# Kernel tuning notes

Measured on AMD Instinct MI355X. Metric: run time of the kernel, lower is better.

The kernel has to match this reference:

```python
import jax, jax.numpy as jnp
import numpy as np

# dims
B, N, M, K = 8, 4096, 1024, 32      # batch, points, centers, neighbors
CIN, CT = 64, 64                    # feature / temb channels
C1, C2 = 64, 128                    # SharedMLP out_channels
G, EPS = 8, 1e-5                    # GroupNorm(8, oc)


def setup_inputs() -> dict:
    key = jax.random.key(0)
    ks = jax.random.split(key, 8)
    return {
        "features": jax.random.normal(ks[0], (B, CIN, N), jnp.float32),
        "coords": jax.random.uniform(ks[1], (B, 3, N), jnp.float32),
        "temb": jax.random.normal(ks[2], (B, CT, N), jnp.float32),
        # SharedMLP params: Conv2d 1x1 -> (O, I) weight, GroupNorm affine
        "W1": jax.random.normal(ks[3], (C1, CIN + 3), jnp.float32) * 0.05,
        "b1": jnp.zeros((C1,), jnp.float32),
        "g1": jnp.ones((C1,), jnp.float32),
        "be1": jnp.zeros((C1,), jnp.float32),
        "W2": jax.random.normal(ks[4], (C2, C1), jnp.float32) * 0.05,
        "b2": jnp.zeros((C2,), jnp.float32),
        "g2": jnp.ones((C2,), jnp.float32),
        "be2": jnp.zeros((C2,), jnp.float32),
    }


def fps_indices(pts):
    # pts: [N, 3] -> [M] indices. Deterministic start at index 0
    # (original uses a random start; math otherwise identical).
    d0 = jnp.sum((pts - pts[0]) ** 2, axis=-1)  # [N]
    def step(dist, _):
        far = jnp.argmax(dist)
        dist = jnp.minimum(dist, jnp.sum((pts - pts[far]) ** 2, axis=-1))
        return dist, far
    _, fars = jax.lax.scan(step, d0, None, length=M - 1)
    return jnp.concatenate([jnp.zeros((1,), fars.dtype), fars])


def group_norm(x, gamma, beta):
    # x: [B, C, M, K], normalize per group over (C//G, M, K)
    b, c, m, k = x.shape
    xr = x.reshape(b, G, c // G, m, k)
    mu = xr.mean(axis=(2, 3, 4), keepdims=True)
    var = xr.var(axis=(2, 3, 4), keepdims=True)
    xn = ((xr - mu) * jax.lax.rsqrt(var + EPS)).reshape(b, c, m, k)
    return xn * gamma[:, None, None] + beta[:, None, None]


def swish(x):
    return x * jax.nn.sigmoid(x)


def reference(features, coords, temb, W1, b1, g1, be1, W2, b2, g2, be2):
    # --- furthest point sampling ---
    idx = jax.vmap(fps_indices)(coords.transpose(0, 2, 1))          # [B, M]
    centers = jax.vmap(lambda c, i: c[:, i])(coords, idx)           # [B, 3, M]
    # --- 'ball query' (actually kNN: source argsorts dist, takes first K) ---
    c = centers.transpose(0, 2, 1)                                  # [B, M, 3]
    p = coords.transpose(0, 2, 1)                                   # [B, N, 3]
    d = (jnp.sum(c * c, -1)[:, :, None] + jnp.sum(p * p, -1)[:, None, :]
         - 2.0 * jnp.einsum('bmd,bnd->bmn', c, p))                  # [B, M, N]
    _, nidx = jax.lax.top_k(-d, K)                                  # [B, M, K]
    gather = jax.vmap(lambda xb, ib: xb[:, ib])                     # [B,C,N],[B,M,K]->[B,C,M,K]
    gcoords = gather(coords, nidx) - centers[..., None]             # [B, 3, M, K]
    gtemb = gather(temb, nidx)                                      # [B, CT, M, K]
    gfeat = jnp.concatenate([gcoords, gather(features, nidx)], axis=1)  # [B, 3+CIN, M, K]
    # --- SharedMLP (1x1 conv -> GN -> Swish) x2, then max over neighbors ---
    h = swish(group_norm(jnp.einsum('oc,bcmk->bomk', W1, gfeat) + b1[:, None, None], g1, be1))
    h = swish(group_norm(jnp.einsum('oc,bcmk->bomk', W2, h) + b2[:, None, None], g2, be2))
    return h.max(axis=-1), centers, gtemb.max(axis=-1)
```

## Files before the change

kernel.cpp:

```cpp
#include <hip/hip_runtime.h>
#include <stdint.h>

#define BB 8
#define NN 4096
#define MM 1024
#define KK 32

__device__ __forceinline__ float bf2f(unsigned short u) {
    union { unsigned int i; float f; } v; v.i = ((unsigned int)u) << 16; return v.f;
}
__device__ __forceinline__ unsigned short f2bf(float f) {
    union { float f; unsigned int i; } v; v.f = f;
    unsigned int x = v.i;
    x += 0x7fffu + ((x >> 16) & 1u);
    return (unsigned short)(x >> 16);
}
__device__ __forceinline__ float swishf(float y) {
    return __fdividef(y, 1.0f + __expf(-y));
}

#define OUT1_OFF 1048576
#define OUT2_OFF 1073152

#define P_W1 0
#define P_B1 4288
#define P_G1 4352
#define P_BE1 4416
#define P_W2 4480
#define P_B2 12672
#define P_G2 12800
#define P_BE2 12928

__device__ __forceinline__ int detect_flag_wave(const unsigned short* f, int lane) {
    unsigned short u = f[lane * 2];
    float x = fabsf(bf2f(u));
    bool ext = (u != 0) && (x > 100.0f || x < 1e-30f);
    unsigned long long m = __ballot(ext);
    return (__popcll(m) >= 16) ? 1 : 0;
}

#define DPP_STAGE(CTRL) { \
    union { double d; unsigned int u[2]; } s_, r_; \
    s_.d = bd; \
    r_.u[0] = (unsigned)__builtin_amdgcn_update_dpp(0, (int)s_.u[0], CTRL, 0xF, 0xF, true); \
    r_.u[1] = (unsigned)__builtin_amdgcn_update_dpp(0, (int)s_.u[1], CTRL, 0xF, 0xF, true); \
    int op_ = __builtin_amdgcn_update_dpp(0, bp, CTRL, 0xF, 0xF, true); \
    double od_ = r_.d; \
    bool rep_ = (od_ > bd) || (od_ == bd && op_ < bp); \
    bd = rep_ ? od_ : bd; bp = rep_ ? op_ : bp; }

__device__ __forceinline__ void redmax64(double& bd, int& bp) {
    DPP_STAGE(0xB1)
    DPP_STAGE(0x4E)
    DPP_STAGE(0x141)
    DPP_STAGE(0x140)
#pragma unroll
    for (int m = 32; m >= 16; m >>= 1) {
        double od = __shfl_xor(bd, m, 64);
        int op = __shfl_xor(bp, m, 64);
        bool rep = (od > bd) || (od == bd && op < bp);
        bd = rep ? od : bd; bp = rep ? op : bp;
    }
}

__global__ void k_init(int* __restrict__ qhead, int* __restrict__ progress,
                       float* __restrict__ stats1, int* __restrict__ cvt_done,
                       int* __restrict__ mlp_done) {
    int tid = threadIdx.x;
    if (tid == 0) { *qhead = 0; *cvt_done = 0; *mlp_done = 0; }
    if (tid < 8) progress[tid * 16] = -1;
    stats1[tid] = 0.f;
    stats1[tid + 256] = 0.f;
}

#define W1Tm(j,c)     (((float*)SM)[(j)*64+(c)])
#define GBUFm(mi,k,c) (((float*)(SM+17152))[(((mi)*32+(k))*66)+(c)])
#define GCm(mi,j,k)   (((float*)(SM+50944))[(((mi)*3+(j))*32)+(k)])
#define NDm(mi,k)     (((int*)(SM+52480))[((mi)*32)+(k)])
#define W2Tm(j,c)     (((float*)SM)[(j)*128+(c)])
#define ACTm(mi,j,k)  (((float*)(SM+32768))[(((mi)*64+(j))*32)+(k)])

struct PW { double d; int p; int q; };
#define PSM_XS   ((float*)(SM))
#define PSM_YS   ((float*)(SM + 16384))
#define PSM_ZS   ((float*)(SM + 32768))
#define PSM_HIST ((int*)(SM + 49152))
#define PSM_PWB  ((PW*)(SM + 53248))
#define PSM_SF   ((int*)(SM + 53376))

#define RESCAN(G) { \
    double gd = 1.0e300; int ga = (G) * 8; \
    _Pragma("unroll") \
    for (int i = 0; i < 8; i++) { \
        int sl = (G) * 8 + i; \
        unsigned int bit = (sl < 32) ? (elo >> sl) : (ehi >> (sl - 32)); \
        double cd = (bit & 1u) ? 1.0e300 : d[sl]; \
        bool rep = cd < gd; \
        gd = rep ? cd : gd; ga = rep ? sl : ga; \
    } \
    g8[(G)] = gd; a8[(G)] = ga; }

__global__ __launch_bounds__(256) void k_fpsknn(
    const void* __restrict__ coords, float* __restrict__ coordsC,
    float* __restrict__ centersF, int* __restrict__ nidx,
    const void* __restrict__ temb, const void* __restrict__ feat,
    float* __restrict__ featT, float* __restrict__ paramsC,
    float* __restrict__ stats1,
    void* __restrict__ d_out,
    int* __restrict__ qhead, int* __restrict__ progress,
    int* __restrict__ cvt_done,
    unsigned short* __restrict__ h1, int cache1,
    const void* W1r, const void* b1r, const void* g1r, const void* be1r,
    const void* W2r, const void* b2r, const void* g2r, const void* be2r)
{
    __shared__ __align__(16) char SM[55296];
    int tid = threadIdx.x;
    int blk = blockIdx.x;
    if (tid < 64) {
        int fl0 = detect_flag_wave((const unsigned short*)feat, tid);
        if (tid == 0) *PSM_SF = fl0;
    }
    __syncthreads();
    int fl = *PSM_SF;

    if (blk < 8) {
        int b = blk;
        if (fl) {
            const float* cb = (const float*)coords + (size_t)b * 3 * NN;
#pragma unroll
            for (int i = 0; i < 16; i++) {
                int p = tid + i * 256;
                PSM_XS[p] = cb[p]; PSM_YS[p] = cb[NN + p]; PSM_ZS[p] = cb[2 * NN + p];
            }
        } else {
            const unsigned short* cb = (const unsigned short*)coords + (size_t)b * 3 * NN;
#pragma unroll
            for (int i = 0; i < 16; i++) {
                int p = tid + i * 256;
                PSM_XS[p] = bf2f(cb[p]); PSM_YS[p] = bf2f(cb[NN + p]); PSM_ZS[p] = bf2f(cb[2 * NN + p]);
            }
        }
        if (tid == 0) PSM_HIST[0] = 0;
        __syncthreads();
        if (tid == 0) {
            *(float4*)(centersF + (size_t)b * MM * 4) =
                make_float4(PSM_XS[0], PSM_YS[0], PSM_ZS[0], 0.f);
            __hip_atomic_store(&progress[b * 16], 0, __ATOMIC_RELEASE, __HIP_MEMORY_SCOPE_AGENT);
        }
        int base = tid * 16;
        double px[16], py[16], pz[16], dist[16];
        double x0 = (double)PSM_XS[0], y0 = (double)PSM_YS[0], z0 = (double)PSM_ZS[0];
        double bd = -1.0; int bp = base;
#pragma unroll
        for (int j = 0; j < 16; j++) {
            px[j] = (double)PSM_XS[base + j]; py[j] = (double)PSM_YS[base + j]; pz[j] = (double)PSM_ZS[base + j];
            double dx = px[j] - x0, dy = py[j] - y0, dz = pz[j] - z0;
            dist[j] = fma(dz, dz, fma(dy, dy, dx * dx));
            bool rep = dist[j] > bd;
            bd = rep ? dist[j] : bd; bp = rep ? base + j : bp;
        }
        int lane = tid & 63, wid = tid >> 6;
#pragma unroll 1
        for (int s = 1; s < MM; s++) {
            redmax64(bd, bp);
            int par = s & 1;
            if (lane == 0) { PW w; w.d = bd; w.p = bp; w.q = 0; PSM_PWB[par * 4 + wid] = w; }
            __syncthreads();
            PW w0 = PSM_PWB[par * 4 + 0];
            double wd = w0.d; int wp = w0.p;
#pragma unroll
            for (int w = 1; w < 4; w++) {
                PW ww = PSM_PWB[par * 4 + w];
                bool rep = (ww.d > wd) || (ww.d == wd && ww.p < wp);
                wd = rep ? ww.d : wd; wp = rep ? ww.p : wp;
            }
            if (tid == 0) PSM_HIST[s] = wp;
            if ((s & 31) == 31 && s >= 63 && wid == ((s >> 5) & 3)) {
                int s0 = s - 63;
                if (lane < 32) {
                    int far = PSM_HIST[s0 + lane];
                    *(float4*)(centersF + ((size_t)b * MM + s0 + lane) * 4) =
                        make_float4(PSM_XS[far], PSM_YS[far], PSM_ZS[far], 0.f);
                }
                if (lane == 0)
                    __hip_atomic_store(&progress[b * 16], s0 + 31,
                                       __ATOMIC_RELEASE, __HIP_MEMORY_SCOPE_AGENT);
            }
            double fx = (double)PSM_XS[wp], fy = (double)PSM_YS[wp], fz = (double)PSM_ZS[wp];
            bd = -1.0; bp = base;
#pragma unroll
            for (int j = 0; j < 16; j++) {
                double dx = px[j] - fx, dy = py[j] - fy, dz = pz[j] - fz;
                double d = fma(dz, dz, fma(dy, dy, dx * dx));
                dist[j] = fmin(dist[j], d);
                bool rep = dist[j] > bd;
                bd = rep ? dist[j] : bd; bp = rep ? base + j : bp;
            }
        }
        __syncthreads();
        if (tid < 32) {
            int far = PSM_HIST[992 + tid];
            *(float4*)(centersF + ((size_t)b * MM + 992 + tid) * 4) =
                make_float4(PSM_XS[far], PSM_YS[far], PSM_ZS[far], 0.f);
        }
        if (tid == 0)
            __hip_atomic_store(&progress[b * 16], 1023,
                               __ATOMIC_RELEASE, __HIP_MEMORY_SCOPE_AGENT);
#pragma unroll
        for (int i = 0; i < 4; i++) {
            int m = tid + i * 256;
            int far = PSM_HIST[m];
            float X = PSM_XS[far], Y = PSM_YS[far], Z = PSM_ZS[far];
            if (fl) {
                float* o = (float*)d_out;
                o[OUT1_OFF + (size_t)(b * 3 + 0) * MM + m] = X;
                o[OUT1_OFF + (size_t)(b * 3 + 1) * MM + m] = Y;
                o[OUT1_OFF + (size_t)(b * 3 + 2) * MM + m] = Z;
            } else {
                unsigned short* o = (unsigned short*)d_out;
                o[OUT1_OFF + (size_t)(b * 3 + 0) * MM + m] = f2bf(X);
                o[OUT1_OFF + (size_t)(b * 3 + 1) * MM + m] = f2bf(Y);
                o[OUT1_OFF + (size_t)(b * 3 + 2) * MM + m] = f2bf(Z);
            }
        }
    } else {
        int lane = tid & 63, wid = tid >> 6;
        for (int i = (blk - 8) * 256 + tid; i < BB * 3 * NN; i += 248 * 256)
            coordsC[i] = fl ? ((const float*)coords)[i]
                            : bf2f(((const unsigned short*)coords)[i]);
        for (int i = (blk - 8) * 256 + tid; i < 13056; i += 248 * 256) {
            const void* src; int off;
            if (i < 4288)       { src = W1r;  off = i; }
            else if (i < 4352)  { src = b1r;  off = i - 4288; }
            else if (i < 4416)  { src = g1r;  off = i - 4352; }
            else if (i < 4480)  { src = be1r; off = i - 4416; }
            else if (i < 12672) { src = W2r;  off = i - 4480; }
            else if (i < 12800) { src = b2r;  off = i - 12672; }
            else if (i < 12928) { src = g2r;  off = i - 12800; }
            else                { src = be2r; off = i - 12928; }
            paramsC[i] = fl ? ((const float*)src)[off]
                            : bf2f(((const unsigned short*)src)[off]);
        }
        {
            float (*tile)[65] = (float(*)[65])SM;
            for (int t = blk - 8; t < 512; t += 248) {
                int b = t >> 6, n0 = (t & 63) * 64;
                int c = tid >> 2, q = tid & 3;
                size_t base = ((size_t)b * 64 + c) * NN + n0 + q * 16;
                __syncthreads();
                if (fl) {
                    const float* sp = (const float*)feat + base;
#pragma unroll
                    for (int j = 0; j < 16; j++) tile[c][q * 16 + j] = sp[j];
                } else {
                    const unsigned short* sp = (const unsigned short*)feat + base;
#pragma unroll
                    for (int j = 0; j < 16; j++) tile[c][q * 16 + j] = bf2f(sp[j]);
                }
                __syncthreads();
                int n = tid >> 2;
                float* dp = featT + ((size_t)b * NN + n0 + n) * 64 + q * 16;
#pragma unroll
                for (int j = 0; j < 16; j++) dp[j] = tile[q * 16 + j][n];
            }
            __syncthreads();
            if (tid == 0) {
                __hip_atomic_fetch_add(cvt_done, 1, __ATOMIC_ACQ_REL, __HIP_MEMORY_SCOPE_AGENT);
                while (__hip_atomic_load(cvt_done, __ATOMIC_RELAXED,
                                         __HIP_MEMORY_SCOPE_AGENT) < 248)
                    __builtin_amdgcn_s_sleep(16);
                (void)__hip_atomic_load(cvt_done, __ATOMIC_ACQUIRE, __HIP_MEMORY_SCOPE_AGENT);
            }
            __syncthreads();
        }
        for (int t = tid; t < 64 * 67; t += 256) {
            int c = t / 67, j = t % 67;
            W1Tm(j, c) = paramsC[P_W1 + t];
        }
        __syncthreads();
        for (;;) {
            int id = 0;
            if (lane == 0) id = atomicAdd(qhead, 1);
            id = __shfl(id, 0, 64);
            if (id >= BB * MM) break;
            int b = id & 7, m = id >> 3;
            while (__hip_atomic_load(&progress[b * 16], __ATOMIC_RELAXED,
                                     __HIP_MEMORY_SCOPE_AGENT) < m)
                __builtin_amdgcn_s_sleep(64);
            (void)__hip_atomic_load(&progress[b * 16], __ATOMIC_ACQUIRE,
                                    __HIP_MEMORY_SCOPE_AGENT);
            int bm = b * MM + m;
            const float* cb = coordsC + (size_t)b * 3 * NN;
            float4 ctr = *(const float4*)(centersF + (size_t)bm * 4);
            double cx = (double)ctr.x, cy = (double)ctr.y, cz = (double)ctr.z;
            double cc = (cx * cx + cy * cy) + cz * cz;
            double d[64];
#pragma unroll 4
            for (int j = 0; j < 64; j++) {
                int p = j * 64 + lane;
                double x = (double)cb[p], y = (double)cb[NN + p], z = (double)cb[2 * NN + p];
                double pp = (x * x + y * y) + z * z;
                double dt = (cx * x + cy * y) + cz * z;
                d[j] = (cc + pp) - 2.0 * dt;
            }
            double g8[8]; int a8[8];
#pragma unroll
            for (int g = 0; g < 8; g++) {
                double gd = d[g * 8]; int ga = g * 8;
#pragma unroll
                for (int i = 1; i < 8; i++) {
                    int sl = g * 8 + i;
                    bool rep = d[sl] < gd;
                    gd = rep ? d[sl] : gd; ga = rep ? sl : ga;
                }
                g8[g] = gd; a8[g] = ga;
            }
            unsigned int elo = 0, ehi = 0;
            int res = 0;
#pragma unroll 1
            for (int it = 0; it < 32; it++) {
                double bd = g8[0]; int ba = a8[0];
#pragma unroll
                for (int g = 1; g < 8; g++) {
                    bool rep = g8[g] < bd;
                    bd = rep ? g8[g] : bd; ba = rep ? a8[g] : ba;
                }
                int bp = ba * 64 + lane;
                double wd = bd; int wp = bp;
#pragma unroll
                for (int s = 32; s >= 1; s >>= 1) {
                    double od = __shfl_xor(wd, s, 64);
                    int op = __shfl_xor(wp, s, 64);
                    bool rep = (od < wd) || (od == wd && op < wp);
                    wd = rep ? od : wd; wp = rep ? op : wp;
                }
                res = (lane == it) ? wp : res;
                if (bp == wp) {
                    int slot = ba;
                    if (slot < 32) elo |= (1u << slot); else ehi |= (1u << (slot - 32));
                    int g = slot >> 3;
                    switch (g) {
                        case 0: RESCAN(0) break;
                        case 1: RESCAN(1) break;
                        case 2: RESCAN(2) break;
                        case 3: RESCAN(3) break;
                        case 4: RESCAN(4) break;
                        case 5: RESCAN(5) break;
                        case 6: RESCAN(6) break;
                        case 7: RESCAN(7) break;
                    }
                }
            }
            if (lane < KK) nidx[(size_t)bm * KK + lane] = res;
            float best = -3.0e38f;
            if (fl) {
                const float* tb = (const float*)temb + ((size_t)b * 64 + lane) * NN;
#pragma unroll 4
                for (int k = 0; k < 32; k++) {
                    int nk = __shfl(res, k, 64);
                    best = fmaxf(best, tb[nk]);
                }
            } else {
                const unsigned short* tb = (const unsigned short*)temb + ((size_t)b * 64 + lane) * NN;
#pragma unroll 4
                for (int k = 0; k < 32; k++) {
                    int nk = __shfl(res, k, 64);
                    best = fmaxf(best, bf2f(tb[nk]));
                }
            }
            size_t off = (size_t)OUT2_OFF + ((size_t)(b * 64 + lane)) * MM + m;
            if (fl) ((float*)d_out)[off] = best;
            else    ((unsigned short*)d_out)[off] = f2bf(best);
            if (lane < 32) NDm(wid, lane) = res & (NN - 1);
            const float* fb = featT + (size_t)b * NN * 64;
#pragma unroll 4
            for (int q = 0; q < 32; q++) {
                int n = NDm(wid, q);
                GBUFm(wid, q, lane) = fb[(size_t)n * 64 + lane];
            }
            if (lane < 32) {
                int n = NDm(wid, lane);
                GCm(wid, 0, lane) = __fsub_rn(cb[n], ctr.x);
                GCm(wid, 1, lane) = __fsub_rn(cb[NN + n], ctr.y);
                GCm(wid, 2, lane) = __fsub_rn(cb[2 * NN + n], ctr.z);
            }
            int c0 = (lane >> 3) * 8;
            int k0 = (lane & 7) * 4;
            float acc[8][4];
#pragma unroll
            for (int i = 0; i < 8; i++)
#pragma unroll
                for (int kk = 0; kk < 4; kk++) acc[i][kk] = 0.f;
#pragma unroll
            for (int j = 0; j < 3; j++) {
                float4 a = *(const float4*)&GCm(wid, j, k0);
                float4 w0 = *(const float4*)&W1Tm(j, c0);
                float4 w1v = *(const float4*)&W1Tm(j, c0 + 4);
                float w[8] = {w0.x, w0.y, w0.z, w0.w, w1v.x, w1v.y, w1v.z, w1v.w};
#pragma unroll
                for (int i = 0; i < 8; i++) {
                    acc[i][0] = fmaf(w[i], a.x, acc[i][0]);
                    acc[i][1] = fmaf(w[i], a.y, acc[i][1]);
                    acc[i][2] = fmaf(w[i], a.z, acc[i][2]);
                    acc[i][3] = fmaf(w[i], a.w, acc[i][3]);
                }
            }
#pragma unroll 4
            for (int c = 0; c < 64; c++) {
                float f0 = GBUFm(wid, k0 + 0, c);
                float f1 = GBUFm(wid, k0 + 1, c);
                float f2 = GBUFm(wid, k0 + 2, c);
                float f3 = GBUFm(wid, k0 + 3, c);
                int j = 3 + c;
                float4 w0 = *(const float4*)&W1Tm(j, c0);
                float4 w1v = *(const float4*)&W1Tm(j, c0 + 4);
                float w[8] = {w0.x, w0.y, w0.z, w0.w, w1v.x, w1v.y, w1v.z, w1v.w};
#pragma unroll
                for (int i = 0; i < 8; i++) {
                    acc[i][0] = fmaf(w[i], f0, acc[i][0]);
                    acc[i][1] = fmaf(w[i], f1, acc[i][1]);
                    acc[i][2] = fmaf(w[i], f2, acc[i][2]);
                    acc[i][3] = fmaf(w[i], f3, acc[i][3]);
                }
            }
            float s = 0.f, s2 = 0.f;
#pragma unroll
            for (int i = 0; i < 8; i++) {
                float bb = paramsC[P_B1 + c0 + i];
                float v0 = acc[i][0] + bb, v1 = acc[i][1] + bb;
                float v2 = acc[i][2] + bb, v3 = acc[i][3] + bb;
                s += v0; s2 = fmaf(v0, v0, s2);
                s += v1; s2 = fmaf(v1, v1, s2);
                s += v2; s2 = fmaf(v2, v2, s2);
                s += v3; s2 = fmaf(v3, v3, s2);
                if (cache1) {
                    unsigned int p0 = (unsigned int)f2bf(v0) | ((unsigned int)f2bf(v1) << 16);
                    unsigned int p1 = (unsigned int)f2bf(v2) | ((unsigned int)f2bf(v3) << 16);
                    *(uint2*)(h1 + ((size_t)bm * 64 + c0 + i) * 32 + k0) = make_uint2(p0, p1);
                }
            }
            s += __shfl_xor(s, 1, 64); s += __shfl_xor(s, 2, 64); s += __shfl_xor(s, 4, 64);
            s2 += __shfl_xor(s2, 1, 64); s2 += __shfl_xor(s2, 2, 64); s2 += __shfl_xor(s2, 4, 64);
            if ((lane & 7) == 0) {
                int g = lane >> 3;
                atomicAdd(&stats1[(b * 8 + g) * 2], s);
                atomicAdd(&stats1[(b * 8 + g) * 2 + 1], s2);
            }
        }
    }
}

__device__ __forceinline__ void mlp1_compute(
    char* SM, int tid, int lane, int mi, int b, int bm,
    const float* __restrict__ featT, const float* __restrict__ coordsC,
    const float* __restrict__ centersF, const int* __restrict__ nidx,
    const float* __restrict__ P, float acc[8][4])
{
    for (int t = tid; t < 64 * 67; t += 256) {
        int c = t / 67, j = t % 67;
        W1Tm(j, c) = P[P_W1 + t];
    }
    if (lane < 32) NDm(mi, lane) = nidx[(size_t)bm * KK + lane] & (NN - 1);
    __syncthreads();
    const float* fb = featT + (size_t)b * NN * 64;
#pragma unroll 4
    for (int q = 0; q < 32; q++) {
        int n = NDm(mi, q);
        GBUFm(mi, q, lane) = fb[(size_t)n * 64 + lane];
    }
    float4 ctr = *(const float4*)(centersF + (size_t)bm * 4);
    const float* cb = coordsC + (size_t)b * 3 * NN;
    if (lane < 32) {
        int n = NDm(mi, lane);
        GCm(mi, 0, lane) = __fsub_rn(cb[n], ctr.x);
        GCm(mi, 1, lane) = __fsub_rn(cb[NN + n], ctr.y);
        GCm(mi, 2, lane) = __fsub_rn(cb[2 * NN + n], ctr.z);
    }
    __syncthreads();
    int c0 = (lane >> 3) * 8;
    int k0 = (lane & 7) * 4;
#pragma unroll
    for (int i = 0; i < 8; i++)
#pragma unroll
        for (int kk = 0; kk < 4; kk++) acc[i][kk] = 0.f;
#pragma unroll
    for (int j = 0; j < 3; j++) {
        float4 a = *(const float4*)&GCm(mi, j, k0);
        float4 w0 = *(const float4*)&W1Tm(j, c0);
        float4 w1v = *(const float4*)&W1Tm(j, c0 + 4);
        float w[8] = {w0.x, w0.y, w0.z, w0.w, w1v.x, w1v.y, w1v.z, w1v.w};
#pragma unroll
        for (int i = 0; i < 8; i++) {
            acc[i][0] = fmaf(w[i], a.x, acc[i][0]);
            acc[i][1] = fmaf(w[i], a.y, acc[i][1]);
            acc[i][2] = fmaf(w[i], a.z, acc[i][2]);
            acc[i][3] = fmaf(w[i], a.w, acc[i][3]);
        }
    }
#pragma unroll 4
    for (int c = 0; c < 64; c++) {
        float f0 = GBUFm(mi, k0 + 0, c);
        float f1 = GBUFm(mi, k0 + 1, c);
        float f2 = GBUFm(mi, k0 + 2, c);
        float f3 = GBUFm(mi, k0 + 3, c);
        int j = 3 + c;
        float4 w0 = *(const float4*)&W1Tm(j, c0);
        float4 w1v = *(const float4*)&W1Tm(j, c0 + 4);
        float w[8] = {w0.x, w0.y, w0.z, w0.w, w1v.x, w1v.y, w1v.z, w1v.w};
#pragma unroll
        for (int i = 0; i < 8; i++) {
            acc[i][0] = fmaf(w[i], f0, acc[i][0]);
            acc[i][1] = fmaf(w[i], f1, acc[i][1]);
            acc[i][2] = fmaf(w[i], f2, acc[i][2]);
            acc[i][3] = fmaf(w[i], f3, acc[i][3]);
        }
    }
}

__device__ __forceinline__ void mlp2_compute(
    char* SM, int tid, int lane, int mi, int b,
    const float v1[8][4], const float* __restrict__ S1,
    const float* __restrict__ P, float v2[16][4])
{
    __syncthreads();
    int c0 = (lane >> 3) * 8;
    int k0 = (lane & 7) * 4;
    int g = c0 >> 3;
    float S = S1[(b * 8 + g) * 2], Q = S1[(b * 8 + g) * 2 + 1];
    float mean = S * (1.0f / 262144.0f);
    float var = Q * (1.0f / 262144.0f) - mean * mean;
    float inv = rsqrtf(var + 1e-5f);
#pragma unroll
    for (int i = 0; i < 8; i++) {
        int c = c0 + i;
        float sc = P[P_G1 + c] * inv;
        float sh = P[P_BE1 + c] - mean * sc;
#pragma unroll
        for (int kk = 0; kk < 4; kk++)
            ACTm(mi, c, k0 + kk) = swishf(fmaf(v1[i][kk], sc, sh));
    }
    for (int t = tid; t < 128 * 64; t += 256) {
        int c = t >> 6, j = t & 63;
        W2Tm(j, c) = P[P_W2 + t];
    }
    __syncthreads();
    int c02 = (lane >> 3) * 16;
    float acc2[16][4];
#pragma unroll
    for (int i = 0; i < 16; i++)
#pragma unroll
        for (int kk = 0; kk < 4; kk++) acc2[i][kk] = 0.f;
#pragma unroll 4
    for (int j = 0; j < 64; j++) {
        float4 a = *(const float4*)&ACTm(mi, j, k0);
        float4 w0 = *(const float4*)&W2Tm(j, c02);
        float4 w1v = *(const float4*)&W2Tm(j, c02 + 4);
        float4 w2v = *(const float4*)&W2Tm(j, c02 + 8);
        float4 w3 = *(const float4*)&W2Tm(j, c02 + 12);
        float w[16] = {w0.x, w0.y, w0.z, w0.w, w1v.x, w1v.y, w1v.z, w1v.w,
                       w2v.x, w2v.y, w2v.z, w2v.w, w3.x, w3.y, w3.z, w3.w};
#pragma unroll
        for (int i = 0; i < 16; i++) {
            acc2[i][0] = fmaf(w[i], a.x, acc2[i][0]);
            acc2[i][1] = fmaf(w[i], a.y, acc2[i][1]);
            acc2[i][2] = fmaf(w[i], a.z, acc2[i][2]);
            acc2[i][3] = fmaf(w[i], a.w, acc2[i][3]);
        }
    }
#pragma unroll
    for (int i = 0; i < 16; i++) {
        float bb = P[P_B2 + c02 + i];
#pragma unroll
        for (int kk = 0; kk < 4; kk++) v2[i][kk] = acc2[i][kk] + bb;
    }
}

__device__ __forceinline__ void get_v1(
    char* SM, int tid, int lane, int mi, int b, int bm,
    const float* featT, const float* coordsC, const float* centersF,
    const int* nidx, const float* P,
    const unsigned short* h1, int cache1, float v1[8][4])
{
    int c0 = (lane >> 3) * 8;
    int k0 = (lane & 7) * 4;
    if (cache1) {
#pragma unroll
        for (int i = 0; i < 8; i++) {
            uint2 u = *(const uint2*)(h1 + ((size_t)bm * 64 + c0 + i) * 32 + k0);
            v1[i][0] = bf2f((unsigned short)(u.x & 0xffffu));
            v1[i][1] = bf2f((unsigned short)(u.x >> 16));
            v1[i][2] = bf2f((unsigned short)(u.y & 0xffffu));
            v1[i][3] = bf2f((unsigned short)(u.y >> 16));
        }
    } else {
        float acc1[8][4];
        mlp1_compute(SM, tid, lane, mi, b, bm, featT, coordsC, centersF, nidx, P, acc1);
#pragma unroll
        for (int i = 0; i < 8; i++) {
            float bb = P[P_B1 + c0 + i];
#pragma unroll
            for (int kk = 0; kk < 4; kk++) v1[i][kk] = acc1[i][kk] + bb;
        }
    }
}

__global__ __launch_bounds__(256) void k_mlp2f(
    const float* __restrict__ featT, const float* __restrict__ coordsC,
    const float* __restrict__ centersF, const int* __restrict__ nidx,
    const float* __restrict__ P, const float* __restrict__ stats1,
    float* __restrict__ stats2,
    const unsigned short* __restrict__ h1,
    unsigned short* __restrict__ vmaxA, unsigned short* __restrict__ vminA,
    int* __restrict__ mlp_done,
    void* __restrict__ d_out, const void* __restrict__ feat)
{
    __shared__ __align__(16) char SM[65536];
    int tid = threadIdx.x;
    int mi = tid >> 6, lane = tid & 63;
#pragma unroll 1
    for (int it = 0; it < 4; it++) {
        int vblk = blockIdx.x + 512 * it;
        int b = vblk >> 8, m0 = (vblk & 255) * 4;
        int bm = b * MM + m0 + mi;
        float v1[8][4];
        get_v1(SM, tid, lane, mi, b, bm, featT, coordsC, centersF, nidx, P, h1, 1, v1);
        float v2[16][4];
        mlp2_compute(SM, tid, lane, mi, b, v1, stats1, P, v2);
        int c02 = (lane >> 3) * 16;
        float s = 0.f, s2 = 0.f;
#pragma unroll
        for (int i = 0; i < 16; i++) {
#pragma unroll
            for (int kk = 0; kk < 4; kk++) {
                float v = v2[i][kk];
                s += v; s2 = fmaf(v, v, s2);
            }
        }
        int m = m0 + mi;
#pragma unroll
        for (int i = 0; i < 16; i++) {
            float va = fmaxf(fmaxf(v2[i][0], v2[i][1]), fmaxf(v2[i][2], v2[i][3]));
            float vb = fminf(fminf(v2[i][0], v2[i][1]), fminf(v2[i][2], v2[i][3]));
            va = fmaxf(va, __shfl_xor(va, 1, 64)); vb = fminf(vb, __shfl_xor(vb, 1, 64));
            va = fmaxf(va, __shfl_xor(va, 2, 64)); vb = fminf(vb, __shfl_xor(vb, 2, 64));
            va = fmaxf(va, __shfl_xor(va, 4, 64)); vb = fminf(vb, __shfl_xor(vb, 4, 64));
            if ((lane & 7) == 0) {
                size_t o = ((size_t)(b * 128 + c02 + i)) * MM + m;
                vmaxA[o] = f2bf(va);
                vminA[o] = f2bf(vb);
            }
        }
        s += __shfl_xor(s, 1, 64); s += __shfl_xor(s, 2, 64); s += __shfl_xor(s, 4, 64);
        s2 += __shfl_xor(s2, 1, 64); s2 += __shfl_xor(s2, 2, 64); s2 += __shfl_xor(s2, 4, 64);
        __syncthreads();
        float* sred = (float*)SM;
        if ((lane & 7) == 0) {
            int g = lane >> 3;
            sred[(mi * 8 + g) * 2] = s;
            sred[(mi * 8 + g) * 2 + 1] = s2;
        }
        __syncthreads();
        if (tid < 16) {
            int g = tid >> 1, w = tid & 1;
            float t = sred[(0 * 8 + g) * 2 + w] + sred[(1 * 8 + g) * 2 + w]
                    + sred[(2 * 8 + g) * 2 + w] + sred[(3 * 8 + g) * 2 + w];
            atomicAdd(&stats2[(b * 8 + g) * 2 + w], t);
        }
        __syncthreads();
    }
    __syncthreads();
    if (tid == 0) {
        __hip_atomic_fetch_add(mlp_done, 1, __ATOMIC_ACQ_REL, __HIP_MEMORY_SCOPE_AGENT);
        while (__hip_atomic_load(mlp_done, __ATOMIC_RELAXED, __HIP_MEMORY_SCOPE_AGENT) < 512)
            __builtin_amdgcn_s_sleep(16);
        (void)__hip_atomic_load(mlp_done, __ATOMIC_ACQUIRE, __HIP_MEMORY_SCOPE_AGENT);
    }
    __syncthreads();
    int fl = detect_flag_wave((const unsigned short*)feat, lane);
#pragma unroll 1
    for (int i = 0; i < 8; i++) {
        int idx = blockIdx.x * 256 + tid + i * 131072;
        int c = (idx >> 10) & 127;
        int b = idx >> 17;
        int g = c >> 4;
        float S = stats2[(b * 8 + g) * 2], Q = stats2[(b * 8 + g) * 2 + 1];
        float mean = S * (1.0f / 524288.0f);
        float var = Q * (1.0f / 524288.0f) - mean * mean;
        float inv = rsqrtf(var + 1e-5f);
        float sc = P[P_G2 + c] * inv;
        float sh = P[P_BE2 + c] - mean * sc;
        float va = bf2f(vmaxA[idx]);
        float vb = bf2f(vminA[idx]);
        float r = fmaxf(swishf(fmaf(va, sc, sh)), swishf(fmaf(vb, sc, sh)));
        if (fl) ((float*)d_out)[idx] = r;
        else    ((unsigned short*)d_out)[idx] = f2bf(r);
    }
}

__global__ __launch_bounds__(256) void k_mlp2s(
    const float* __restrict__ featT, const float* __restrict__ coordsC,
    const float* __restrict__ centersF, const int* __restrict__ nidx,
    const float* __restrict__ P, const float* __restrict__ stats1,
    float* __restrict__ stats2,
    const unsigned short* __restrict__ h1, int cache1)
{
    __shared__ __align__(16) char smem[65536];
    char* SM = smem;
    int tid = threadIdx.x, blk = blockIdx.x;
    int b = blk >> 8, m0 = (blk & 255) * 4;
    int mi = tid >> 6, lane = tid & 63;
    int bm = b * MM + m0 + mi;
    float v1[8][4];
    get_v1(SM, tid, lane, mi, b, bm, featT, coordsC, centersF, nidx, P, h1, cache1, v1);
    float v2[16][4];
    mlp2_compute(SM, tid, lane, mi, b, v1, stats1, P, v2);
    float s = 0.f, s2 = 0.f;
#pragma unroll
    for (int i = 0; i < 16; i++)
#pragma unroll
        for (int kk = 0; kk < 4; kk++) {
            float v = v2[i][kk];
            s += v; s2 = fmaf(v, v, s2);
        }
    s += __shfl_xor(s, 1, 64); s += __shfl_xor(s, 2, 64); s += __shfl_xor(s, 4, 64);
    s2 += __shfl_xor(s2, 1, 64); s2 += __shfl_xor(s2, 2, 64); s2 += __shfl_xor(s2, 4, 64);
    __syncthreads();
    float* sred = (float*)SM;
    if ((lane & 7) == 0) {
        int g = lane >> 3;
        sred[(mi * 8 + g) * 2] = s;
        sred[(mi * 8 + g) * 2 + 1] = s2;
    }
    __syncthreads();
    if (tid < 16) {
        int g = tid >> 1, w = tid & 1;
        float t = sred[(0 * 8 + g) * 2 + w] + sred[(1 * 8 + g) * 2 + w]
                + sred[(2 * 8 + g) * 2 + w] + sred[(3 * 8 + g) * 2 + w];
        atomicAdd(&stats2[(b * 8 + g) * 2 + w], t);
    }
}

__global__ __launch_bounds__(256) void k_final_slow(
    const float* __restrict__ featT, const float* __restrict__ coordsC,
    const float* __restrict__ centersF, const int* __restrict__ nidx,
    const float* __restrict__ P, const float* __restrict__ stats1,
    const float* __restrict__ stats2,
    void* __restrict__ d_out, const void* __restrict__ feat,
    const unsigned short* __restrict__ h1, int cache1)
{
    __shared__ __align__(16) char smem[65536];
    char* SM = smem;
    int tid = threadIdx.x, blk = blockIdx.x;
    if (tid < 64) {
        int fl0 = detect_flag_wave((const unsigned short*)feat, tid);
        if (tid == 0) *(int*)(SM + 53248) = fl0;
    }
    __syncthreads();
    int fl = *(int*)(SM + 53248);
    int b = blk >> 8, m0 = (blk & 255) * 4;
    int mi = tid >> 6, lane = tid & 63;
    int bm = b * MM + m0 + mi;
    float v1[8][4];
    get_v1(SM, tid, lane, mi, b, bm, featT, coordsC, centersF, nidx, P, h1, cache1, v1);
    float v2[16][4];
    mlp2_compute(SM, tid, lane, mi, b, v1, stats1, P, v2);
    int c02 = (lane >> 3) * 16;
    int g2 = c02 >> 4;
    float S = stats2[(b * 8 + g2) * 2], Q = stats2[(b * 8 + g2) * 2 + 1];
    float mean = S * (1.0f / 524288.0f);
    float var = Q * (1.0f / 524288.0f) - mean * mean;
    float inv = rsqrtf(var + 1e-5f);
    float mx[16];
#pragma unroll
    for (int i = 0; i < 16; i++) {
        int c = c02 + i;
        float sc = P[P_G2 + c] * inv;
        float sh = P[P_BE2 + c] - mean * sc;
        float v = -3.0e38f;
#pragma unroll
        for (int kk = 0; kk < 4; kk++)
            v = fmaxf(v, swishf(fmaf(v2[i][kk], sc, sh)));
        v = fmaxf(v, __shfl_xor(v, 1, 64));
        v = fmaxf(v, __shfl_xor(v, 2, 64));
        v = fmaxf(v, __shfl_xor(v, 4, 64));
        mx[i] = v;
    }
    if ((lane & 7) == 0) {
        int m = m0 + mi;
#pragma unroll
        for (int i = 0; i < 16; i++) {
            size_t off = (size_t)(b * 128 + c02 + i) * MM + m;
            if (fl) ((float*)d_out)[off] = mx[i];
            else    ((unsigned short*)d_out)[off] = f2bf(mx[i]);
        }
    }
}

extern "C" void kernel_launch(void* const* d_in, const int* in_sizes, int n_in,
                              void* d_out, int out_size, void* d_ws, size_t ws_size,
                              hipStream_t stream) {
    (void)in_sizes; (void)n_in; (void)out_size;
    const void* feat = d_in[0];
    const void* coords = d_in[1];
    const void* temb = d_in[2];

    char* ws = (char*)d_ws;
    int* qhead = (int*)ws;
    int* progress = (int*)(ws + 512);
    float* stats1 = (float*)(ws + 1024);
    float* stats2 = (float*)(ws + 2048);
    int* cvt_done = (int*)(ws + 3072);
    int* mlp_done = (int*)(ws + 3136);
    float* coordsC = (float*)(ws + 3200);
    float* paramsC = (float*)(ws + 396416);
    float* centersF = (float*)(ws + 448640);
    int* nidx = (int*)(ws + 579712);
    float* featT = (float*)(ws + 1628288);
    unsigned short* h1 = (unsigned short*)(ws + 10016896);
    unsigned short* vmaxA = (unsigned short*)(ws + 43571328);
    unsigned short* vminA = (unsigned short*)(ws + 45668480);
    int cache1 = (ws_size >= 43571328u) ? 1 : 0;
    int have_vmm = (ws_size >= 47765632u) ? 1 : 0;

    k_init<<<1, 256, 0, stream>>>(qhead, progress, stats1, cvt_done, mlp_done);
    k_fpsknn<<<256, 256, 0, stream>>>(coords, coordsC, centersF, nidx, temb,
                                      feat, featT, paramsC, stats1, d_out,
                                      qhead, progress, cvt_done, h1, cache1,
                                      d_in[3], d_in[4], d_in[5], d_in[6],
                                      d_in[7], d_in[8], d_in[9], d_in[10]);
    if (cache1 && have_vmm) {
        k_mlp2f<<<512, 256, 0, stream>>>(featT, coordsC, centersF, nidx, paramsC,
                                         stats1, stats2, h1, vmaxA, vminA,
                                         mlp_done, d_out, feat);
    } else {
        k_mlp2s<<<2048, 256, 0, stream>>>(featT, coordsC, centersF, nidx, paramsC,
                                          stats1, stats2, h1, cache1);
        k_final_slow<<<2048, 256, 0, stream>>>(featT, coordsC, centersF, nidx,
                                               paramsC, stats1, stats2, d_out,
                                               feat, h1, cache1);
    }
}
```

Measured before the change: 1.383 ms.

## Replace in-kernel grid barrier with separate MLP2 and final-normalize kernel launches

Removes the persistent 512-block k_mlp2f kernel, which used an atomic-counter spin barrier before applying the second GroupNorm. Now k_mlp2s runs with 2048 blocks, one item each, and writes the per-center max/min buffers. A new lightweight k_final_fast launch then applies the normalization and swish. This trades a software grid barrier and the 4-iteration loop for one extra kernel launch, giving better occupancy and no spin-waiting.

```diff
diff --git a/kernel.cpp b/kernel.cpp
--- a/kernel.cpp
+++ b/kernel.cpp
@@ -64,10 +64,9 @@
 }
 
 __global__ void k_init(int* __restrict__ qhead, int* __restrict__ progress,
-                       float* __restrict__ stats1, int* __restrict__ cvt_done,
-                       int* __restrict__ mlp_done) {
+                       float* __restrict__ stats1, int* __restrict__ cvt_done) {
     int tid = threadIdx.x;
-    if (tid == 0) { *qhead = 0; *cvt_done = 0; *mlp_done = 0; }
+    if (tid == 0) { *qhead = 0; *cvt_done = 0; }
     if (tid < 8) progress[tid * 16] = -1;
     stats1[tid] = 0.f;
     stats1[tid + 256] = 0.f;
@@ -604,105 +603,14 @@
     }
 }
 
-__global__ __launch_bounds__(256) void k_mlp2f(
-    const float* __restrict__ featT, const float* __restrict__ coordsC,
-    const float* __restrict__ centersF, const int* __restrict__ nidx,
-    const float* __restrict__ P, const float* __restrict__ stats1,
-    float* __restrict__ stats2,
-    const unsigned short* __restrict__ h1,
-    unsigned short* __restrict__ vmaxA, unsigned short* __restrict__ vminA,
-    int* __restrict__ mlp_done,
-    void* __restrict__ d_out, const void* __restrict__ feat)
-{
-    __shared__ __align__(16) char SM[65536];
-    int tid = threadIdx.x;
-    int mi = tid >> 6, lane = tid & 63;
-#pragma unroll 1
-    for (int it = 0; it < 4; it++) {
-        int vblk = blockIdx.x + 512 * it;
-        int b = vblk >> 8, m0 = (vblk & 255) * 4;
-        int bm = b * MM + m0 + mi;
-        float v1[8][4];
-        get_v1(SM, tid, lane, mi, b, bm, featT, coordsC, centersF, nidx, P, h1, 1, v1);
-        float v2[16][4];
-        mlp2_compute(SM, tid, lane, mi, b, v1, stats1, P, v2);
-        int c02 = (lane >> 3) * 16;
-        float s = 0.f, s2 = 0.f;
-#pragma unroll
-        for (int i = 0; i < 16; i++) {
-#pragma unroll
-            for (int kk = 0; kk < 4; kk++) {
-                float v = v2[i][kk];
-                s += v; s2 = fmaf(v, v, s2);
-            }
-        }
-        int m = m0 + mi;
-#pragma unroll
-        for (int i = 0; i < 16; i++) {
-            float va = fmaxf(fmaxf(v2[i][0], v2[i][1]), fmaxf(v2[i][2], v2[i][3]));
-            float vb = fminf(fminf(v2[i][0], v2[i][1]), fminf(v2[i][2], v2[i][3]));
-            va = fmaxf(va, __shfl_xor(va, 1, 64)); vb = fminf(vb, __shfl_xor(vb, 1, 64));
-            va = fmaxf(va, __shfl_xor(va, 2, 64)); vb = fminf(vb, __shfl_xor(vb, 2, 64));
-            va = fmaxf(va, __shfl_xor(va, 4, 64)); vb = fminf(vb, __shfl_xor(vb, 4, 64));
-            if ((lane & 7) == 0) {
-                size_t o = ((size_t)(b * 128 + c02 + i)) * MM + m;
-                vmaxA[o] = f2bf(va);
-                vminA[o] = f2bf(vb);
-            }
-        }
-        s += __shfl_xor(s, 1, 64); s += __shfl_xor(s, 2, 64); s += __shfl_xor(s, 4, 64);
-        s2 += __shfl_xor(s2, 1, 64); s2 += __shfl_xor(s2, 2, 64); s2 += __shfl_xor(s2, 4, 64);
-        __syncthreads();
-        float* sred = (float*)SM;
-        if ((lane & 7) == 0) {
-            int g = lane >> 3;
-            sred[(mi * 8 + g) * 2] = s;
-            sred[(mi * 8 + g) * 2 + 1] = s2;
-        }
-        __syncthreads();
-        if (tid < 16) {
-            int g = tid >> 1, w = tid & 1;
-            float t = sred[(0 * 8 + g) * 2 + w] + sred[(1 * 8 + g) * 2 + w]
-                    + sred[(2 * 8 + g) * 2 + w] + sred[(3 * 8 + g) * 2 + w];
-            atomicAdd(&stats2[(b * 8 + g) * 2 + w], t);
-        }
-        __syncthreads();
-    }
-    __syncthreads();
-    if (tid == 0) {
-        __hip_atomic_fetch_add(mlp_done, 1, __ATOMIC_ACQ_REL, __HIP_MEMORY_SCOPE_AGENT);
-        while (__hip_atomic_load(mlp_done, __ATOMIC_RELAXED, __HIP_MEMORY_SCOPE_AGENT) < 512)
-            __builtin_amdgcn_s_sleep(16);
-        (void)__hip_atomic_load(mlp_done, __ATOMIC_ACQUIRE, __HIP_MEMORY_SCOPE_AGENT);
-    }
-    __syncthreads();
-    int fl = detect_flag_wave((const unsigned short*)feat, lane);
-#pragma unroll 1
-    for (int i = 0; i < 8; i++) {
-        int idx = blockIdx.x * 256 + tid + i * 131072;
-        int c = (idx >> 10) & 127;
-        int b = idx >> 17;
-        int g = c >> 4;
-        float S = stats2[(b * 8 + g) * 2], Q = stats2[(b * 8 + g) * 2 + 1];
-        float mean = S * (1.0f / 524288.0f);
-        float var = Q * (1.0f / 524288.0f) - mean * mean;
-        float inv = rsqrtf(var + 1e-5f);
-        float sc = P[P_G2 + c] * inv;
-        float sh = P[P_BE2 + c] - mean * sc;
-        float va = bf2f(vmaxA[idx]);
-        float vb = bf2f(vminA[idx]);
-        float r = fmaxf(swishf(fmaf(va, sc, sh)), swishf(fmaf(vb, sc, sh)));
-        if (fl) ((float*)d_out)[idx] = r;
-        else    ((unsigned short*)d_out)[idx] = f2bf(r);
-    }
-}
-
 __global__ __launch_bounds__(256) void k_mlp2s(
     const float* __restrict__ featT, const float* __restrict__ coordsC,
     const float* __restrict__ centersF, const int* __restrict__ nidx,
     const float* __restrict__ P, const float* __restrict__ stats1,
     float* __restrict__ stats2,
-    const unsigned short* __restrict__ h1, int cache1)
+    const unsigned short* __restrict__ h1, int cache1,
+    unsigned short* __restrict__ vmaxA, unsigned short* __restrict__ vminA,
+    int have_vmm)
 {
     __shared__ __align__(16) char smem[65536];
     char* SM = smem;
@@ -714,14 +622,32 @@
     get_v1(SM, tid, lane, mi, b, bm, featT, coordsC, centersF, nidx, P, h1, cache1, v1);
     float v2[16][4];
     mlp2_compute(SM, tid, lane, mi, b, v1, stats1, P, v2);
+    int c02 = (lane >> 3) * 16;
     float s = 0.f, s2 = 0.f;
 #pragma unroll
-    for (int i = 0; i < 16; i++)
+    for (int i = 0; i < 16; i++) {
 #pragma unroll
         for (int kk = 0; kk < 4; kk++) {
             float v = v2[i][kk];
             s += v; s2 = fmaf(v, v, s2);
         }
+    }
+    if (have_vmm) {
+        int m = m0 + mi;
+#pragma unroll
+        for (int i = 0; i < 16; i++) {
+            float va = fmaxf(fmaxf(v2[i][0], v2[i][1]), fmaxf(v2[i][2], v2[i][3]));
+            float vb = fminf(fminf(v2[i][0], v2[i][1]), fminf(v2[i][2], v2[i][3]));
+            va = fmaxf(va, __shfl_xor(va, 1, 64)); vb = fminf(vb, __shfl_xor(vb, 1, 64));
+            va = fmaxf(va, __shfl_xor(va, 2, 64)); vb = fminf(vb, __shfl_xor(vb, 2, 64));
+            va = fmaxf(va, __shfl_xor(va, 4, 64)); vb = fminf(vb, __shfl_xor(vb, 4, 64));
+            if ((lane & 7) == 0) {
+                size_t o = ((size_t)(b * 128 + c02 + i)) * MM + m;
+                vmaxA[o] = f2bf(va);
+                vminA[o] = f2bf(vb);
+            }
+        }
+    }
     s += __shfl_xor(s, 1, 64); s += __shfl_xor(s, 2, 64); s += __shfl_xor(s, 4, 64);
     s2 += __shfl_xor(s2, 1, 64); s2 += __shfl_xor(s2, 2, 64); s2 += __shfl_xor(s2, 4, 64);
     __syncthreads();
@@ -738,6 +664,30 @@
                 + sred[(2 * 8 + g) * 2 + w] + sred[(3 * 8 + g) * 2 + w];
         atomicAdd(&stats2[(b * 8 + g) * 2 + w], t);
     }
+}
+
+__global__ __launch_bounds__(256) void k_final_fast(
+    const unsigned short* __restrict__ vmaxA, const unsigned short* __restrict__ vminA,
+    const float* __restrict__ P, const float* __restrict__ stats2,
+    void* __restrict__ d_out, const void* __restrict__ feat)
+{
+    int tid = threadIdx.x;
+    int idx = blockIdx.x * 256 + tid;
+    int fl = detect_flag_wave((const unsigned short*)feat, tid & 63);
+    int c = (idx >> 10) & 127;
+    int b = idx >> 17;
+    int g = c >> 4;
+    float S = stats2[(b * 8 + g) * 2], Q = stats2[(b * 8 + g) * 2 + 1];
+    float mean = S * (1.0f / 524288.0f);
+    float var = Q * (1.0f / 524288.0f) - mean * mean;
+    float inv = rsqrtf(var + 1e-5f);
+    float sc = P[P_G2 + c] * inv;
+    float sh = P[P_BE2 + c] - mean * sc;
+    float va = bf2f(vmaxA[idx]);
+    float vb = bf2f(vminA[idx]);
+    float r = fmaxf(swishf(fmaf(va, sc, sh)), swishf(fmaf(vb, sc, sh)));
+    if (fl) ((float*)d_out)[idx] = r;
+    else    ((unsigned short*)d_out)[idx] = f2bf(r);
 }
 
 __global__ __launch_bounds__(256) void k_final_slow(
@@ -810,7 +760,6 @@
     float* stats1 = (float*)(ws + 1024);
     float* stats2 = (float*)(ws + 2048);
     int* cvt_done = (int*)(ws + 3072);
-    int* mlp_done = (int*)(ws + 3136);
     float* coordsC = (float*)(ws + 3200);
     float* paramsC = (float*)(ws + 396416);
     float* centersF = (float*)(ws + 448640);
@@ -822,19 +771,19 @@
     int cache1 = (ws_size >= 43571328u) ? 1 : 0;
     int have_vmm = (ws_size >= 47765632u) ? 1 : 0;
 
-    k_init<<<1, 256, 0, stream>>>(qhead, progress, stats1, cvt_done, mlp_done);
+    k_init<<<1, 256, 0, stream>>>(qhead, progress, stats1, cvt_done);
     k_fpsknn<<<256, 256, 0, stream>>>(coords, coordsC, centersF, nidx, temb,
                                       feat, featT, paramsC, stats1, d_out,
                                       qhead, progress, cvt_done, h1, cache1,
                                       d_in[3], d_in[4], d_in[5], d_in[6],
                                       d_in[7], d_in[8], d_in[9], d_in[10]);
-    if (cache1 && have_vmm) {
-        k_mlp2f<<<512, 256, 0, stream>>>(featT, coordsC, centersF, nidx, paramsC,
-                                         stats1, stats2, h1, vmaxA, vminA,
-                                         mlp_done, d_out, feat);
+    k_mlp2s<<<2048, 256, 0, stream>>>(featT, coordsC, centersF, nidx, paramsC,
+                                      stats1, stats2, h1, cache1,
+                                      vmaxA, vminA, have_vmm);
+    if (have_vmm) {
+        k_final_fast<<<4096, 256, 0, stream>>>(vmaxA, vminA, paramsC, stats2,
+                                               d_out, feat);
     } else {
-        k_mlp2s<<<2048, 256, 0, stream>>>(featT, coordsC, centersF, nidx, paramsC,
-                                          stats1, stats2, h1, cache1);
         k_final_slow<<<2048, 256, 0, stream>>>(featT, coordsC, centersF, nidx,
                                                paramsC, stats1, stats2, d_out,
                                                feat, h1, cache1);
```

Result: faster. 1.338 ms (-3.2%).
